# Optimization experiments

Hardware: AMD Instinct MI355X
Metric: run time of the kernel (lower is better)

Reference implementation:

```python
import jax, jax.numpy as jnp
import numpy as np

DIM = 512
HEADS = 8
DHEAD = DIM // 8          # 64
INNER = HEADS * DHEAD     # 512
M_LANDMARKS = 256
PINV_ITERS = 6
KSZ = 33                  # residual depthwise conv kernel (default)


def setup_inputs() -> dict:
    key = jax.random.key(0)
    ks = jax.random.split(key, 5)
    B, N = 1, 16384
    s = DIM ** -0.5
    return {
        "x": jax.random.normal(ks[0], (B, N, DIM), jnp.float32),
        "norm_w": jnp.ones((DIM,), jnp.float32),
        "norm_b": jnp.zeros((DIM,), jnp.float32),
        "w_qkv": jax.random.normal(ks[1], (3 * INNER, DIM), jnp.float32) * s,   # Linear(dim, 3*inner, bias=False)
        "w_out": jax.random.normal(ks[2], (DIM, INNER), jnp.float32) * s,        # Linear(inner, dim)
        "b_out": jnp.zeros((DIM,), jnp.float32),
        "conv_w": jax.random.normal(ks[3], (HEADS, 1, KSZ, 1), jnp.float32) * 0.1,  # depthwise Conv2d(h,h,(33,1),groups=h)
    }


def _layernorm(x, w, b, eps=1e-5):
    mu = x.mean(-1, keepdims=True)
    var = ((x - mu) ** 2).mean(-1, keepdims=True)
    return (x - mu) * jax.lax.rsqrt(var + eps) * w + b


def _moore_penrose_pinv(a, iters):
    # a: [B, H, m, m]; matches lucidrains moore_penrose_iter_pinv (global max over col/row sums)
    abs_a = jnp.abs(a)
    col = abs_a.sum(-1).max()
    row = abs_a.sum(-2).max()
    z = jnp.swapaxes(a, -1, -2) / (col * row)
    I = jnp.eye(a.shape[-1], dtype=a.dtype)
    for _ in range(iters):
        az = a @ z
        z = 0.25 * z @ (13 * I - az @ (15 * I - az @ (7 * I - az)))
    return z


def _nystrom_attention(h, w_qkv, w_out, b_out, conv_w):
    B, N, _ = h.shape
    qkv = h @ w_qkv.T                          # [B, N, 3*inner]
    q, k, v = jnp.split(qkv, 3, axis=-1)

    def heads(t):
        return t.reshape(B, N, HEADS, DHEAD).transpose(0, 2, 1, 3)  # [B, H, N, d]
    q = heads(q) * (DHEAD ** -0.5)
    k = heads(k)
    v = heads(v)

    # landmark pooling: mean over contiguous groups of size l = N / m
    l = N // M_LANDMARKS
    q_l = q.reshape(B, HEADS, M_LANDMARKS, l, DHEAD).mean(3)   # [B, H, m, d]
    k_l = k.reshape(B, HEADS, M_LANDMARKS, l, DHEAD).mean(3)

    attn1 = jax.nn.softmax(jnp.einsum('bhnd,bhmd->bhnm', q, k_l), axis=-1)      # [B,H,N,m]
    attn2 = jax.nn.softmax(jnp.einsum('bhid,bhjd->bhij', q_l, k_l), axis=-1)    # [B,H,m,m]
    attn3 = jax.nn.softmax(jnp.einsum('bhmd,bhnd->bhmn', q_l, k), axis=-1)      # [B,H,m,N]

    attn2_inv = _moore_penrose_pinv(attn2, PINV_ITERS)
    out = attn1 @ (attn2_inv @ (attn3 @ v))                                     # [B,H,N,d]

    # residual depthwise conv along sequence dim (kernel 33x1, groups=HEADS, no bias)
    conv = jax.lax.conv_general_dilated(
        v, conv_w, window_strides=(1, 1),
        padding=((KSZ // 2, KSZ // 2), (0, 0)),
        dimension_numbers=('NCHW', 'OIHW', 'NCHW'),
        feature_group_count=HEADS)
    out = out + conv

    out = out.transpose(0, 2, 1, 3).reshape(B, N, INNER)
    return out @ w_out.T + b_out


def reference(x, norm_w, norm_b, w_qkv, w_out, b_out, conv_w):
    h = _layernorm(x, norm_w, norm_b)
    return x + _nystrom_attention(h, w_qkv, w_out, b_out, conv_w)
```

## Files before the change

### kernel.cpp

```cpp
#include <hip/hip_runtime.h>
#include <hip/hip_bf16.h>


typedef __attribute__((ext_vector_type(8))) short bf16x8;
typedef __attribute__((ext_vector_type(4))) float f32x4;

#define MFMA16(A, B, C) __builtin_amdgcn_mfma_f32_16x16x32_bf16(A, B, C, 0, 0, 0)
#define GLD16(g, l) __builtin_amdgcn_global_load_lds( \
    (const __attribute__((address_space(1))) void*)(g), \
    (__attribute__((address_space(3))) void*)(l), 16, 0, 0)

static __device__ __forceinline__ unsigned short f2b(float f) {
  __hip_bfloat16 h = __float2bfloat16(f);
  return *reinterpret_cast<unsigned short*>(&h);
}
static __device__ __forceinline__ float b2f(unsigned short u) {
  return __uint_as_float(((unsigned)u) << 16);
}

#define FMA16(ACC, AV, BV) do { \
  ACC[0][0] += AV.x*BV.x; ACC[0][1] += AV.x*BV.y; ACC[0][2] += AV.x*BV.z; ACC[0][3] += AV.x*BV.w; \
  ACC[1][0] += AV.y*BV.x; ACC[1][1] += AV.y*BV.y; ACC[1][2] += AV.y*BV.z; ACC[1][3] += AV.y*BV.w; \
  ACC[2][0] += AV.z*BV.x; ACC[2][1] += AV.z*BV.y; ACC[2][2] += AV.z*BV.z; ACC[2][3] += AV.z*BV.w; \
  ACC[3][0] += AV.w*BV.x; ACC[3][1] += AV.w*BV.y; ACC[3][2] += AV.w*BV.z; ACC[3][3] += AV.w*BV.w; \
} while (0)

__global__ __launch_bounds__(256) void k_init(const float* __restrict__ x,
    const float* __restrict__ nw, const float* __restrict__ nb,
    unsigned short* __restrict__ h,
    const float* __restrict__ wq, unsigned short* __restrict__ wqb,
    const float* __restrict__ wo, unsigned short* __restrict__ wob) {
  const int b = blockIdx.x;
  const int t = threadIdx.x;
  if (b < 8192) {
    const int row = b * 2 + (t >> 7);
    const int tl = t & 127;
    const float4 xv = ((const float4*)(x + (size_t)row * 512))[tl];
    float s  = xv.x + xv.y + xv.z + xv.w;
    float sq = xv.x*xv.x + xv.y*xv.y + xv.z*xv.z + xv.w*xv.w;
    #pragma unroll
    for (int o = 32; o > 0; o >>= 1) {
      s  += __shfl_down(s, o, 64);
      sq += __shfl_down(sq, o, 64);
    }
    __shared__ float ls[4], lq[4];
    if ((t & 63) == 0) { ls[t >> 6] = s; lq[t >> 6] = sq; }
    __syncthreads();
    const int base = (t >> 7) << 1;
    s = ls[base] + ls[base + 1]; sq = lq[base] + lq[base + 1];
    const float mean = s * (1.0f / 512.0f);
    const float var  = sq * (1.0f / 512.0f) - mean * mean;
    const float rstd = rsqrtf(var + 1e-5f);
    const float4 wv = ((const float4*)nw)[tl];
    const float4 bv = ((const float4*)nb)[tl];
    ushort4 hv;
    hv.x = f2b((xv.x - mean) * rstd * wv.x + bv.x);
    hv.y = f2b((xv.y - mean) * rstd * wv.y + bv.y);
    hv.z = f2b((xv.z - mean) * rstd * wv.z + bv.z);
    hv.w = f2b((xv.w - mean) * rstd * wv.w + bv.w);
    ((ushort4*)(h + (size_t)row * 512))[tl] = hv;
  } else if (b < 8960) {
    const int i = (b - 8192) * 256 + t;
    const float4 f = ((const float4*)wq)[i];
    ushort4 u;
    u.x = f2b(f.x); u.y = f2b(f.y); u.z = f2b(f.z); u.w = f2b(f.w);
    ((ushort4*)wqb)[i] = u;
  } else {
    const int i = (b - 8960) * 256 + t;
    const float4 f = ((const float4*)wo)[i];
    ushort4 u;
    u.x = f2b(f.x); u.y = f2b(f.y); u.z = f2b(f.z); u.w = f2b(f.w);
    ((ushort4*)wob)[i] = u;
  }
}

__device__ __forceinline__ void stage_tile(const unsigned short* __restrict__ A,
    const unsigned short* __restrict__ B, unsigned short* lds,
    int m0, int n0, int k0, int tid) {
  #pragma unroll
  for (int c = 0; c < 2; ++c) {
    const int s = c * 512 + tid;
    const int grow = ((s >> 6) << 4) | (s & 15);
    const int chunk = (s >> 4) & 3;
    GLD16(A + (size_t)(m0 + grow) * 512 + k0 + chunk * 8, lds + s * 8);
    GLD16(B + (size_t)(n0 + grow) * 512 + k0 + chunk * 8, lds + 8192 + s * 8);
  }
}

__device__ __forceinline__ void compute_tile(const unsigned short* lds,
    f32x4 (&acc)[8][4], int wr, int wc, int quad, int l15) {
  bf16x8 a[8], b[4];
  #pragma unroll
  for (int i = 0; i < 8; ++i)
    a[i] = *(const bf16x8*)(lds + (size_t)((wr * 8 + i) * 64 + quad * 16 + l15) * 8);
  #pragma unroll
  for (int j = 0; j < 4; ++j)
    b[j] = *(const bf16x8*)(lds + 8192 + (size_t)((wc * 4 + j) * 64 + quad * 16 + l15) * 8);
  __builtin_amdgcn_s_setprio(1);
  #pragma unroll
  for (int i = 0; i < 8; ++i)
    #pragma unroll
    for (int j = 0; j < 4; ++j)
      acc[i][j] = MFMA16(a[i], b[j], acc[i][j]);
  __builtin_amdgcn_s_setprio(0);
}

#define GEMM256_PIPELINE(Aptr, Bptr, M0, N0)                                 \
  f32x4 acc[8][4];                                                           \
  _Pragma("unroll")                                                          \
  for (int i = 0; i < 8; ++i)                                                \
    _Pragma("unroll")                                                        \
    for (int j = 0; j < 4; ++j) acc[i][j] = (f32x4){0.f, 0.f, 0.f, 0.f};     \
  stage_tile(Aptr, Bptr, lds, M0, N0, 0, tid);                               \
  asm volatile("" ::: "memory");                                             \
  stage_tile(Aptr, Bptr, lds + 16384, M0, N0, 32, tid);                      \
  asm volatile("s_waitcnt vmcnt(4)" ::: "memory");                           \
  __builtin_amdgcn_s_barrier();                                              \
  for (int t = 0; t < 14; ++t) {                                             \
    compute_tile(lds + (t & 1) * 16384, acc, wr, wc, quad, l15);             \
    asm volatile("" ::: "memory");                                           \
    __builtin_amdgcn_s_barrier();       \
    asm volatile("" ::: "memory");                                           \
    stage_tile(Aptr, Bptr, lds + (t & 1) * 16384, M0, N0, (t + 2) * 32, tid);\
    asm volatile("s_waitcnt vmcnt(4)" ::: "memory");    \
    __builtin_amdgcn_s_barrier();                                            \
  }                                                                          \
  compute_tile(lds, acc, wr, wc, quad, l15);             \
  asm volatile("s_waitcnt vmcnt(0)" ::: "memory");                           \
  __builtin_amdgcn_s_barrier();                                              \
  compute_tile(lds + 16384, acc, wr, wc, quad, l15);

__global__ __launch_bounds__(512) void k_qkv2(const unsigned short* __restrict__ A,
    const unsigned short* __restrict__ B,
    unsigned short* __restrict__ qb, unsigned short* __restrict__ kb,
    unsigned short* __restrict__ vb) {
  __shared__ __align__(16) unsigned short lds[32768];
  const int tid = threadIdx.x;
  const int lane = tid & 63, w = tid >> 6;
  const int wr = w >> 2, wc = w & 3;
  const int quad = lane >> 4, l15 = lane & 15;
  const int bid = blockIdx.x;
  const int swz = (bid & 7) * 48 + (bid >> 3);
  const int by = swz / 6, bx = swz - by * 6;
  const int m0 = by * 256, n0 = bx * 256;

  GEMM256_PIPELINE(A, B, m0, n0)

  const int part = n0 >> 9;
  const int head = ((n0 & 511) >> 6) + wc;
  unsigned short* dst = (part == 0) ? qb : (part == 1) ? kb : vb;
  const float scale = (part == 0) ? 0.125f : 1.0f;
  unsigned short* dp = dst + (size_t)head * 16384 * 64;
  #pragma unroll
  for (int i = 0; i < 8; ++i) {
    const int rowb = m0 + wr * 128 + i * 16 + quad * 4;
    #pragma unroll
    for (int j = 0; j < 4; ++j) {
      const int dd = j * 16 + l15;
      #pragma unroll
      for (int r = 0; r < 4; ++r)
        dp[(size_t)(rowb + r) * 64 + dd] = f2b(acc[i][j][r] * scale);
    }
  }
}

__global__ __launch_bounds__(256) void k_tr(const unsigned short* __restrict__ v,
    unsigned short* __restrict__ vt) {
  __shared__ unsigned short T[64][72];
  const int t = threadIdx.x;
  const int n0 = blockIdx.x * 64, h = blockIdx.y;
  const int n = t >> 2, sg = (t & 3) * 16;
  const unsigned short* p = v + ((size_t)(h * 16384 + n0 + n)) * 64 + sg;
  #pragma unroll
  for (int i = 0; i < 16; i += 4) {
    const ushort4 u = *(const ushort4*)(p + i);
    T[sg + i + 0][n] = u.x; T[sg + i + 1][n] = u.y;
    T[sg + i + 2][n] = u.z; T[sg + i + 3][n] = u.w;
  }
  __syncthreads();
  const int d = t >> 2, so = (t & 3) * 16;
  unsigned short* q = vt + ((size_t)(h * 64 + d)) * 16384 + n0 + so;
  #pragma unroll
  for (int i = 0; i < 16; i += 4) {
    ushort4 u;
    u.x = T[d][so + i]; u.y = T[d][so + i + 1];
    u.z = T[d][so + i + 2]; u.w = T[d][so + i + 3];
    *(ushort4*)(q + i) = u;
  }
}

__global__ __launch_bounds__(256) void k_landmark(const unsigned short* __restrict__ qb,
    const unsigned short* __restrict__ kb, float* __restrict__ qlf,
    unsigned short* __restrict__ qlb, float* __restrict__ klf,
    unsigned short* __restrict__ klb) {
  const int t = threadIdx.x, d = t & 63, grp = t >> 6;
  const int m = blockIdx.x, h = blockIdx.y;
  const unsigned short* src = blockIdx.z ? kb : qb;
  const unsigned short* p = src + ((size_t)h * 16384 + m * 64 + grp * 16) * 64 + d;
  float s = 0.f;
  #pragma unroll
  for (int i = 0; i < 16; ++i) s += b2f(p[(size_t)i * 64]);
  __shared__ float red[4][64];
  red[grp][d] = s;
  __syncthreads();
  if (t < 64) {
    float v = (red[0][d] + red[1][d]) + (red[2][d] + red[3][d]);
    v *= (1.0f / 64.0f);
    const size_t oi = ((size_t)h * 256 + m) * 64 + d;
    if (blockIdx.z == 0) { qlf[oi] = v; qlb[oi] = f2b(v); }
    else                 { klf[oi] = v; klb[oi] = f2b(v); }
  }
}

__global__ __launch_bounds__(256) void k_attn2(const float* __restrict__ ql,
    const float* __restrict__ kl, float* __restrict__ a2, unsigned short* __restrict__ a2b,
    float* __restrict__ csum) {
  const int i = blockIdx.x, h = blockIdx.y, j = threadIdx.x;
  __shared__ float qrow[64];
  __shared__ float wred[4];
  __shared__ float wsum[4];
  if (j < 64) qrow[j] = ql[((size_t)h * 256 + i) * 64 + j];
  __syncthreads();
  const float* kr = kl + ((size_t)h * 256 + j) * 64;
  float s = 0.f;
  #pragma unroll 8
  for (int d = 0; d < 64; ++d) s += qrow[d] * kr[d];
  float mx = s;
  #pragma unroll
  for (int o2 = 32; o2 > 0; o2 >>= 1) mx = fmaxf(mx, __shfl_xor(mx, o2, 64));
  if ((j & 63) == 0) wred[j >> 6] = mx;
  __syncthreads();
  mx = fmaxf(fmaxf(wred[0], wred[1]), fmaxf(wred[2], wred[3]));
  const float e = __expf(s - mx);
  float sm = e;
  #pragma unroll
  for (int o2 = 32; o2 > 0; o2 >>= 1) sm += __shfl_xor(sm, o2, 64);
  if ((j & 63) == 0) wsum[j >> 6] = sm;
  __syncthreads();
  sm = wsum[0] + wsum[1] + wsum[2] + wsum[3];
  const float v = e / sm;
  const size_t idx = ((size_t)h * 256 + i) * 256 + j;
  a2[idx] = v;
  a2b[idx] = f2b(v);
  atomicAdd(&csum[h * 256 + j], v);
}

__global__ __launch_bounds__(256) void k_z0(const float* __restrict__ a2,
    const float* __restrict__ csum, unsigned short* __restrict__ z0b,
    unsigned short* __restrict__ z0t) {
  __shared__ float T[64][65];
  __shared__ float wm[4];
  const int bi = blockIdx.x, bj = blockIdx.y, h = blockIdx.z;
  const int t = threadIdx.x;
  const int r = t >> 2, cseg = (t & 3) * 16;
  float m = 0.f;
  #pragma unroll
  for (int c = 0; c < 8; ++c) m = fmaxf(m, csum[c * 256 + t]);
  #pragma unroll
  for (int o2 = 32; o2 > 0; o2 >>= 1) m = fmaxf(m, __shfl_xor(m, o2, 64));
  if ((t & 63) == 0) wm[t >> 6] = m;
  __syncthreads();
  const float g = fmaxf(fmaxf(wm[0], wm[1]), fmaxf(wm[2], wm[3]));
  const float inv = 1.0f / g;
  const float* p = a2 + ((size_t)h * 256 + bj * 64 + r) * 256 + bi * 64 + cseg;
  unsigned short* qt = z0t + ((size_t)h * 256 + bj * 64 + r) * 256 + bi * 64 + cseg;
  #pragma unroll
  for (int i = 0; i < 16; i += 4) {
    const float4 f = *(const float4*)(p + i);
    T[cseg + i + 0][r] = f.x; T[cseg + i + 1][r] = f.y;
    T[cseg + i + 2][r] = f.z; T[cseg + i + 3][r] = f.w;
    ushort4 u;
    u.x = f2b(f.x * inv); u.y = f2b(f.y * inv);
    u.z = f2b(f.z * inv); u.w = f2b(f.w * inv);
    *(ushort4*)(qt + i) = u;
  }
  __syncthreads();
  unsigned short* qb_ = z0b + ((size_t)h * 256 + bi * 64 + r) * 256 + bj * 64 + cseg;
  #pragma unroll
  for (int i = 0; i < 16; i += 4) {
    ushort4 u;
    u.x = f2b(T[r][cseg + i] * inv);     u.y = f2b(T[r][cseg + i + 1] * inv);
    u.z = f2b(T[r][cseg + i + 2] * inv); u.w = f2b(T[r][cseg + i + 3] * inv);
    *(ushort4*)(qb_ + i) = u;
  }
}

__global__ __launch_bounds__(256) void k_pgemm(const unsigned short* __restrict__ A,
    const unsigned short* __restrict__ Bt, unsigned short* __restrict__ Cn,
    unsigned short* __restrict__ Ct, float* __restrict__ Cf,
    float alpha, float sdiag, int use_diag) {
  __shared__ unsigned short As[64 * 128];
  __shared__ unsigned short Bs[64 * 128];
  const int t = threadIdx.x;
  const int lane = t & 63, w = t >> 6;
  const int quad = lane >> 4, l15 = lane & 15;
  const int bn = blockIdx.x, bm = blockIdx.y, h = blockIdx.z;
  const size_t hs = (size_t)h * 65536;
  const unsigned short* Ap = A + hs + (size_t)(bm * 64) * 256;
  const unsigned short* Bp = Bt + hs + (size_t)(bn * 64) * 256;
  f32x4 acc[4];
  #pragma unroll
  for (int j = 0; j < 4; ++j) acc[j] = (f32x4){0.f, 0.f, 0.f, 0.f};
  for (int kh = 0; kh < 2; ++kh) {
    __syncthreads();
    #pragma unroll
    for (int c = 0; c < 4; ++c) {
      const int slot = c * 256 + t;
      const int row = slot >> 4, pc = slot & 15;
      const int lc = pc ^ (row & 7);
      GLD16(Ap + (size_t)row * 256 + kh * 128 + lc * 8, As + slot * 8);
      GLD16(Bp + (size_t)row * 256 + kh * 128 + lc * 8, Bs + slot * 8);
    }
    __syncthreads();
    #pragma unroll
    for (int kc = 0; kc < 4; ++kc) {
      const int arow = w * 16 + l15;
      const bf16x8 a = *(const bf16x8*)(As + arow * 128 + ((kc * 4 + quad) ^ (arow & 7)) * 8);
      #pragma unroll
      for (int j = 0; j < 4; ++j) {
        const int brow = j * 16 + l15;
        const bf16x8 b = *(const bf16x8*)(Bs + brow * 128 + ((kc * 4 + quad) ^ (brow & 7)) * 8);
        acc[j] = MFMA16(a, b, acc[j]);
      }
    }
  }
  const int row0 = bm * 64 + w * 16 + quad * 4;
  #pragma unroll
  for (int j = 0; j < 4; ++j) {
    const int col = bn * 64 + j * 16 + l15;
    float v[4];
    #pragma unroll
    for (int r = 0; r < 4; ++r) v[r] = acc[j][r] * alpha;
    if (Cn) {
      #pragma unroll
      for (int r = 0; r < 4; ++r) Cn[hs + (size_t)(row0 + r) * 256 + col] = f2b(v[r]);
    }
    if (Cf) {
      #pragma unroll
      for (int r = 0; r < 4; ++r) Cf[hs + (size_t)(row0 + r) * 256 + col] = v[r];
    }
    ushort4 u;
    float tv[4];
    #pragma unroll
    for (int r = 0; r < 4; ++r)
      tv[r] = use_diag ? ((col == row0 + r ? sdiag : 0.f) - v[r]) : v[r];
    u.x = f2b(tv[0]); u.y = f2b(tv[1]); u.z = f2b(tv[2]); u.w = f2b(tv[3]);
    *(ushort4*)(Ct + hs + (size_t)col * 256 + row0) = u;
  }
}

__global__ __launch_bounds__(256) void k_gemm256(const float* __restrict__ A,
    const float* __restrict__ B, float* __restrict__ C,
    int lda, int ldb, int ldc,
    unsigned long long sA, unsigned long long sB, unsigned long long sC,
    float alpha, float sdiag, int use_diag,
    const float* __restrict__ rs, unsigned long long sRS) {
  A += (size_t)blockIdx.z * sA;
  B += (size_t)blockIdx.z * sB;
  C += (size_t)blockIdx.z * sC;
  if (rs) rs += (size_t)blockIdx.z * sRS;
  __shared__ float As[16][68];
  __shared__ float Bs[16][68];
  const int t = threadIdx.x, tx = t & 15, ty = t >> 4;
  const int bn = blockIdx.x, bm = blockIdx.y;
  const int lr = t >> 2, lk = (t & 3) << 2;
  const int bkr = t >> 4, bnc = (t & 15) << 2;
  float acc[4][4] = {{0.f}};
  for (int k0 = 0; k0 < 256; k0 += 16) {
    float4 a4 = *(const float4*)(A + (size_t)(bm * 64 + lr) * lda + k0 + lk);
    float4 b4 = *(const float4*)(B + (size_t)(k0 + bkr) * ldb + bn * 64 + bnc);
    if (use_diag) {
      const int kg = k0 + bkr, ngb = bn * 64 + bnc;
      b4.x = (kg == ngb + 0 ? sdiag : 0.f) - b4.x;
      b4.y = (kg == ngb + 1 ? sdiag : 0.f) - b4.y;
      b4.z = (kg == ngb + 2 ? sdiag : 0.f) - b4.z;
      b4.w = (kg == ngb + 3 ? sdiag : 0.f) - b4.w;
    }
    if (rs) {
      const float rv = 1.0f / rs[k0 + bkr];
      b4.x *= rv; b4.y *= rv; b4.z *= rv; b4.w *= rv;
    }
    __syncthreads();
    As[lk+0][lr] = a4.x; As[lk+1][lr] = a4.y; As[lk+2][lr] = a4.z; As[lk+3][lr] = a4.w;
    *(float4*)&Bs[bkr][bnc] = b4;
    __syncthreads();
    #pragma unroll
    for (int kq = 0; kq < 16; ++kq) {
      const float4 av = *(const float4*)&As[kq][ty << 2];
      const float4 bv = *(const float4*)&Bs[kq][tx << 2];
      FMA16(acc, av, bv);
    }
  }
  #pragma unroll
  for (int ii = 0; ii < 4; ++ii)
    #pragma unroll
    for (int jj = 0; jj < 4; ++jj)
      C[(size_t)(bm * 64 + (ty << 2) + ii) * ldc + bn * 64 + (tx << 2) + jj] =
          alpha * acc[ii][jj];
}

__global__ __launch_bounds__(256) void k_gemmD(const float* __restrict__ A,
    const float* __restrict__ B, const float* __restrict__ rs,
    unsigned short* __restrict__ dtb) {
  __shared__ float Asf[16 * 68];
  __shared__ float Bsf[16 * 68];
  const int bm = blockIdx.x, h = blockIdx.y;
  A += (size_t)h * 65536;
  B += (size_t)h * 16384;
  rs += (size_t)h * 256;
  const int t = threadIdx.x, tx = t & 15, ty = t >> 4;
  const int lr = t >> 2, lk = (t & 3) << 2;
  const int bkr = t >> 4, bnc = (t & 15) << 2;
  float acc[4][4] = {{0.f}};
  for (int k0 = 0; k0 < 256; k0 += 16) {
    float4 a4 = *(const float4*)(A + (size_t)(bm * 64 + lr) * 256 + k0 + lk);
    float4 b4 = *(const float4*)(B + (size_t)(k0 + bkr) * 64 + bnc);
    const float rv = 1.0f / rs[k0 + bkr];
    b4.x *= rv; b4.y *= rv; b4.z *= rv; b4.w *= rv;
    __syncthreads();
    Asf[(lk + 0) * 68 + lr] = a4.x; Asf[(lk + 1) * 68 + lr] = a4.y;
    Asf[(lk + 2) * 68 + lr] = a4.z; Asf[(lk + 3) * 68 + lr] = a4.w;
    *(float4*)&Bsf[bkr * 68 + bnc] = b4;
    __syncthreads();
    #pragma unroll
    for (int kq = 0; kq < 16; ++kq) {
      const float4 av = *(const float4*)&Asf[kq * 68 + (ty << 2)];
      const float4 bv = *(const float4*)&Bsf[kq * 68 + (tx << 2)];
      FMA16(acc, av, bv);
    }
  }
  #pragma unroll
  for (int ii = 0; ii < 4; ++ii)
    #pragma unroll
    for (int jj = 0; jj < 4; ++jj)
      dtb[(size_t)(h * 64 + (tx << 2) + jj) * 256 + bm * 64 + (ty << 2) + ii] =
          f2b(acc[ii][jj]);
}

__global__ __launch_bounds__(256) void k_w3_mfma(const unsigned short* __restrict__ qlb,
    const unsigned short* __restrict__ kb, const unsigned short* __restrict__ vt,
    float* __restrict__ W, float* __restrict__ lsum) {
  __shared__ unsigned short QLs[64 * 64];
  __shared__ unsigned short Ks [64 * 64];
  __shared__ unsigned short Vts[64 * 64];
  __shared__ unsigned short Ps [64 * 64];
  const int t = threadIdx.x;
  const int lane = t & 63, w = t >> 6;
  const int quad = lane >> 4, l15 = lane & 15;
  const int kc = blockIdx.x, mt = blockIdx.y, h = blockIdx.z;
  #pragma unroll
  for (int c = 0; c < 2; ++c) {
    const int slot = c * 256 + t;
    const int row = slot >> 3, pc = slot & 7, lc = pc ^ (row & 7);
    GLD16(qlb + ((size_t)(h * 256 + mt * 64 + row)) * 64 + lc * 8, QLs + slot * 8);
  }
  __syncthreads();
  const int arow = w * 16 + l15;
  const bf16x8 aq0 = *(const bf16x8*)(QLs + arow * 64 + ((quad    ) ^ (arow & 7)) * 8);
  const bf16x8 aq1 = *(const bf16x8*)(QLs + arow * 64 + ((quad + 4) ^ (arow & 7)) * 8);
  f32x4 wacc[4];
  #pragma unroll
  for (int dt = 0; dt < 4; ++dt) wacc[dt] = (f32x4){0.f, 0.f, 0.f, 0.f};
  float lacc[4] = {0.f, 0.f, 0.f, 0.f};
  for (int ss = 0; ss < 16; ++ss) {
    const int n0 = kc * 1024 + ss * 64;
    __syncthreads();
    #pragma unroll
    for (int c = 0; c < 2; ++c) {
      const int slot = c * 256 + t;
      const int row = slot >> 3, pc = slot & 7, lc = pc ^ (row & 7);
      GLD16(kb + ((size_t)(h * 16384 + n0 + row)) * 64 + lc * 8, Ks + slot * 8);
      GLD16(vt + ((size_t)(h * 64 + row)) * 16384 + n0 + lc * 8, Vts + slot * 8);
    }
    __syncthreads();
    f32x4 s[4];
    #pragma unroll
    for (int j = 0; j < 4; ++j) {
      s[j] = (f32x4){0.f, 0.f, 0.f, 0.f};
      const int brow = j * 16 + l15;
      const bf16x8 b0 = *(const bf16x8*)(Ks + brow * 64 + ((quad    ) ^ (brow & 7)) * 8);
      const bf16x8 b1 = *(const bf16x8*)(Ks + brow * 64 + ((quad + 4) ^ (brow & 7)) * 8);
      s[j] = MFMA16(aq0, b0, s[j]);
      s[j] = MFMA16(aq1, b1, s[j]);
    }
    #pragma unroll
    for (int j = 0; j < 4; ++j)
      #pragma unroll
      for (int r = 0; r < 4; ++r) {
        const float e = __expf(s[j][r]);
        lacc[r] += e;
        const int prow = w * 16 + quad * 4 + r, pcol = j * 16 + l15;
        Ps[prow * 64 + (((pcol >> 3) ^ (prow & 7)) << 3) + (pcol & 7)] = f2b(e);
      }
    __syncthreads();
    const bf16x8 ap0 = *(const bf16x8*)(Ps + arow * 64 + ((quad    ) ^ (arow & 7)) * 8);
    const bf16x8 ap1 = *(const bf16x8*)(Ps + arow * 64 + ((quad + 4) ^ (arow & 7)) * 8);
    #pragma unroll
    for (int dt = 0; dt < 4; ++dt) {
      const int brow = dt * 16 + l15;
      const bf16x8 b0 = *(const bf16x8*)(Vts + brow * 64 + ((quad    ) ^ (brow & 7)) * 8);
      const bf16x8 b1 = *(const bf16x8*)(Vts + brow * 64 + ((quad + 4) ^ (brow & 7)) * 8);
      wacc[dt] = MFMA16(ap0, b0, wacc[dt]);
      wacc[dt] = MFMA16(ap1, b1, wacc[dt]);
    }
  }
  #pragma unroll
  for (int dt = 0; dt < 4; ++dt)
    #pragma unroll
    for (int r = 0; r < 4; ++r)
      atomicAdd(&W[((size_t)(h * 256 + mt * 64 + w * 16 + quad * 4 + r)) * 64 + dt * 16 + l15],
                wacc[dt][r]);
// ... 47 lines not shown
  __syncthreads();
  f32x4 cacc[4];
  #pragma unroll
  for (int dt = 0; dt < 4; ++dt) cacc[dt] = (f32x4){0.f, 0.f, 0.f, 0.f};
  #pragma unroll
  for (int kcc = 0; kcc < 3; ++kcc) {
    const bf16x8 a = *(const bf16x8*)(Wb + arow * 96 + (((kcc * 4 + quad) ^ (arow & 3)) << 3));
    int off = n0 - 16 + kcc * 32 + quad * 8;
    off = off < 0 ? 0 : (off > 16376 ? 16376 : off);
    #pragma unroll
    for (int dt = 0; dt < 4; ++dt) {
      const bf16x8 b = *(const bf16x8*)(vt + ((size_t)(h * 64 + dt * 16 + l15)) * 16384 + off);
      cacc[dt] = MFMA16(a, b, cacc[dt]);
    }
  }
  f32x4 oacc[4];
  #pragma unroll
  for (int dt = 0; dt < 4; ++dt) oacc[dt] = (f32x4){0.f, 0.f, 0.f, 0.f};
  float lacc[4] = {0.f, 0.f, 0.f, 0.f};
  for (int mc = 0; mc < 4; ++mc) {
    const int m0 = mc * 64;
    __syncthreads();
    #pragma unroll
    for (int c = 0; c < 2; ++c) {
      const int slot = c * 256 + t;
      const int row = slot >> 3, pc = slot & 7, lc = pc ^ (row & 7);
      GLD16(klb + ((size_t)(h * 256 + m0 + row)) * 64 + lc * 8, Ks + slot * 8);
      GLD16(dtb + ((size_t)(h * 64 + row)) * 256 + m0 + lc * 8, Ds + slot * 8);
    }
    __syncthreads();
    f32x4 s[4];
    #pragma unroll
    for (int j = 0; j < 4; ++j) {
      s[j] = (f32x4){0.f, 0.f, 0.f, 0.f};
      const int brow = j * 16 + l15;
      const bf16x8 b0 = *(const bf16x8*)(Ks + brow * 64 + ((quad    ) ^ (brow & 7)) * 8);
      const bf16x8 b1 = *(const bf16x8*)(Ks + brow * 64 + ((quad + 4) ^ (brow & 7)) * 8);
      s[j] = MFMA16(aq0, b0, s[j]);
      s[j] = MFMA16(aq1, b1, s[j]);
    }
    #pragma unroll
    for (int j = 0; j < 4; ++j)
      #pragma unroll
      for (int r = 0; r < 4; ++r) {
        const float e = __expf(s[j][r]);
        lacc[r] += e;
        const int prow = w * 16 + quad * 4 + r, pcol = j * 16 + l15;
        Ps[prow * 64 + (((pcol >> 3) ^ (prow & 7)) << 3) + (pcol & 7)] = f2b(e);
      }
    __syncthreads();
    const bf16x8 ap0 = *(const bf16x8*)(Ps + arow * 64 + ((quad    ) ^ (arow & 7)) * 8);
    const bf16x8 ap1 = *(const bf16x8*)(Ps + arow * 64 + ((quad + 4) ^ (arow & 7)) * 8);
    #pragma unroll
    for (int dt = 0; dt < 4; ++dt) {
      const int brow = dt * 16 + l15;
      const bf16x8 b0 = *(const bf16x8*)(Ds + brow * 64 + ((quad    ) ^ (brow & 7)) * 8);
      const bf16x8 b1 = *(const bf16x8*)(Ds + brow * 64 + ((quad + 4) ^ (brow & 7)) * 8);
      oacc[dt] = MFMA16(ap0, b0, oacc[dt]);
      oacc[dt] = MFMA16(ap1, b1, oacc[dt]);
    }
  }
  #pragma unroll
  for (int r = 0; r < 4; ++r)
    #pragma unroll
    for (int msk = 1; msk < 16; msk <<= 1) lacc[r] += __shfl_xor(lacc[r], msk, 64);
  #pragma unroll
  for (int dt = 0; dt < 4; ++dt)
    #pragma unroll
    for (int r = 0; r < 4; ++r) {
      const float val = oacc[dt][r] / lacc[r] + cacc[dt][r];
      o[((size_t)(n0 + w * 16 + quad * 4 + r)) * 512 + h * 64 + dt * 16 + l15] = f2b(val);
    }
}

__global__ __launch_bounds__(256) void k_out_mfma(const unsigned short* __restrict__ A,
    const unsigned short* __restrict__ B, const float* __restrict__ bias,
    const float* __restrict__ xres, float* __restrict__ out) {
  __shared__ unsigned short As[128 * 32];
  __shared__ unsigned short Bs[128 * 32];
  const int t = threadIdx.x;
  const int lane = t & 63, w = t >> 6;
  const int quad = lane >> 4, l15 = lane & 15;
  const int wm = (w >> 1) * 64, wn = (w & 1) * 64;
  const int m0 = blockIdx.y * 128, n0 = blockIdx.x * 128;
  f32x4 acc[4][4];
  #pragma unroll
  for (int i = 0; i < 4; ++i)
    #pragma unroll
    for (int j = 0; j < 4; ++j) acc[i][j] = (f32x4){0.f, 0.f, 0.f, 0.f};
  for (int k0 = 0; k0 < 512; k0 += 32) {
    __syncthreads();
    #pragma unroll
    for (int c = 0; c < 2; ++c) {
      const int slot = c * 256 + t;
      const int row = slot >> 2, seg = slot & 3;
      GLD16(A + (size_t)(m0 + row) * 512 + k0 + seg * 8, As + slot * 8);
      GLD16(B + (size_t)(n0 + row) * 512 + k0 + seg * 8, Bs + slot * 8);
    }
    __syncthreads();
    bf16x8 a[4], b[4];
    #pragma unroll
    for (int i = 0; i < 4; ++i)
      a[i] = *(const bf16x8*)(As + (wm + i * 16 + l15) * 32 + quad * 8);
    #pragma unroll
    for (int j = 0; j < 4; ++j)
      b[j] = *(const bf16x8*)(Bs + (wn + j * 16 + l15) * 32 + quad * 8);
    #pragma unroll
    for (int i = 0; i < 4; ++i)
      #pragma unroll
      for (int j = 0; j < 4; ++j)
        acc[i][j] = MFMA16(a[i], b[j], acc[i][j]);
  }
  #pragma unroll
  for (int i = 0; i < 4; ++i)
    #pragma unroll
    for (int j = 0; j < 4; ++j)
      #pragma unroll
      for (int r = 0; r < 4; ++r) {
        const int row = m0 + wm + i * 16 + quad * 4 + r;
        const int col = n0 + wn + j * 16 + l15;
        out[(size_t)row * 512 + col] = acc[i][j][r] + bias[col] + xres[(size_t)row * 512 + col];
      }
}

extern "C" void kernel_launch(void* const* d_in, const int* in_sizes, int n_in,
                              void* d_out, int out_size, void* d_ws, size_t ws_size,
                              hipStream_t stream) {
  const float* x      = (const float*)d_in[0];
  const float* norm_w = (const float*)d_in[1];
  const float* norm_b = (const float*)d_in[2];
  const float* w_qkv  = (const float*)d_in[3];
  const float* w_out  = (const float*)d_in[4];
  const float* b_out  = (const float*)d_in[5];
  const float* conv_w = (const float*)d_in[6];
  float* out = (float*)d_out;

  char* cur = (char*)d_ws;
  auto alloc = [&](size_t bytes) -> char* {
    char* p = cur;
    cur += (bytes + 255) & ~(size_t)255;
    return p;
  };
  const size_t NB = (size_t)16384 * 512;
  const size_t LM = (size_t)8 * 256 * 64;
  const size_t SQ = (size_t)8 * 256 * 256;

  unsigned short* h_b  = (unsigned short*)alloc(NB * 2);
  unsigned short* wq_b = (unsigned short*)alloc((size_t)1536 * 512 * 2);
  unsigned short* wo_b = (unsigned short*)alloc((size_t)512 * 512 * 2);
  unsigned short* qb   = (unsigned short*)alloc(NB * 2);
  unsigned short* kb   = (unsigned short*)alloc(NB * 2);
  unsigned short* vb   = (unsigned short*)alloc(NB * 2);
  unsigned short* vt   = (unsigned short*)alloc(NB * 2);
  float*          qlf  = (float*)alloc(LM * 4);
  float*          klf  = (float*)alloc(LM * 4);
  unsigned short* qlb  = (unsigned short*)alloc(LM * 2);
  unsigned short* klb  = (unsigned short*)alloc(LM * 2);
  float*          a2   = (float*)alloc(SQ * 4);
  unsigned short* a2b  = (unsigned short*)alloc(SQ * 2);
  unsigned short* z0b  = (unsigned short*)alloc(SQ * 2);
  unsigned short* z0t  = (unsigned short*)alloc(SQ * 2);
  unsigned short* Pn   = (unsigned short*)alloc(SQ * 2);
  unsigned short* Pt   = (unsigned short*)alloc(SQ * 2);
  unsigned short* Q1t  = (unsigned short*)alloc(SQ * 2);
  unsigned short* Q2t  = (unsigned short*)alloc(SQ * 2);
  unsigned short* zp0n = (unsigned short*)alloc(SQ * 2);
  unsigned short* zp0t = (unsigned short*)alloc(SQ * 2);
  unsigned short* zp1n = (unsigned short*)alloc(SQ * 2);
  unsigned short* zp1t = (unsigned short*)alloc(SQ * 2);
  float*          zf5  = (float*)alloc(SQ * 4);
  float*          zfin = (float*)alloc(SQ * 4);
  float*          Pp   = (float*)alloc(SQ * 4);
  float*          Q1   = (float*)alloc(SQ * 4);
  float*          Q2   = (float*)alloc(SQ * 4);
  float*          W    = (float*)alloc(LM * 4 + 4096 * 4);
  float*          lsum = W + LM;
  float*          csum = W + LM + 2048;
  unsigned short* dtb  = (unsigned short*)alloc(LM * 2);
  unsigned short* o_b  = (unsigned short*)alloc(NB * 2);

  hipMemsetAsync(W, 0, (LM + 4096) * sizeof(float), stream);
  k_init<<<9216, 256, 0, stream>>>(x, norm_w, norm_b, h_b, w_qkv, wq_b, w_out, wo_b);
  k_qkv2<<<384, 512, 0, stream>>>(h_b, wq_b, qb, kb, vb);
  k_tr<<<dim3(256, 8), 256, 0, stream>>>(vb, vt);
  k_landmark<<<dim3(256, 8, 2), 256, 0, stream>>>(qb, kb, qlf, qlb, klf, klb);
  k_attn2<<<dim3(256, 8), 256, 0, stream>>>(qlf, klf, a2, a2b, csum);
  k_z0<<<dim3(4, 4, 8), 256, 0, stream>>>(a2, csum, z0b, z0t);
  k_w3_mfma<<<dim3(16, 4, 8), 256, 0, stream>>>(qlb, kb, vt, W, lsum);

  unsigned short* zan = z0b; unsigned short* zat = z0t;
  for (int it = 0; it < 5; ++it) {
    unsigned short* zbn = (it & 1) ? zp1n : zp0n;
    unsigned short* zbt = (it & 1) ? zp1t : zp0t;
    k_pgemm<<<dim3(4, 4, 8), 256, 0, stream>>>(a2b, zat, Pn, Pt, nullptr, 1.f, 7.f, 1);
    k_pgemm<<<dim3(4, 4, 8), 256, 0, stream>>>(Pn, Pt, nullptr, Q1t, nullptr, 1.f, 15.f, 1);
    k_pgemm<<<dim3(4, 4, 8), 256, 0, stream>>>(Pn, Q1t, nullptr, Q2t, nullptr, 1.f, 13.f, 1);
    k_pgemm<<<dim3(4, 4, 8), 256, 0, stream>>>(zan, Q2t, zbn, zbt,
        it == 4 ? zf5 : nullptr, 0.25f, 0.f, 0);
    zan = zbn; zat = zbt;
  }
  k_gemm256<<<dim3(4, 4, 8), 256, 0, stream>>>(a2, zf5, Pp, 256, 256, 256,
      65536ULL, 65536ULL, 65536ULL, 1.f, 0.f, 0, nullptr, 0ULL);
  k_gemm256<<<dim3(4, 4, 8), 256, 0, stream>>>(Pp, Pp, Q1, 256, 256, 256,
      65536ULL, 65536ULL, 65536ULL, 1.f, 7.f, 1, nullptr, 0ULL);
  k_gemm256<<<dim3(4, 4, 8), 256, 0, stream>>>(Pp, Q1, Q2, 256, 256, 256,
      65536ULL, 65536ULL, 65536ULL, 1.f, 15.f, 1, nullptr, 0ULL);
  k_gemm256<<<dim3(4, 4, 8), 256, 0, stream>>>(zf5, Q2, zfin, 256, 256, 256,
      65536ULL, 65536ULL, 65536ULL, 0.25f, 13.f, 1, nullptr, 0ULL);

  k_gemmD<<<dim3(4, 8), 256, 0, stream>>>(zfin, W, lsum, dtb);

  k_attn1_mfma<<<dim3(256, 8), 256, 0, stream>>>(qb, klb, dtb, vt, conv_w, o_b);
  k_out_mfma<<<dim3(4, 128), 256, 0, stream>>>(o_b, wo_b, b_out, x, out);
}
```

Before: 446.8 us.

## Retile QKV GEMM, fuse transpose with landmark pooling, halve pinv GEMM tiles

Replaces the 256x256 double-buffered QKV GEMM with a simpler 128x128 single-buffered MFMA kernel that uses an XCD-aware block mapping. The V transpose and the landmark pooling are merged into one launch. The pinv GEMMs (bf16 MFMA and fp32) switch to 64x32 tiles, doubling block count so the small matrices fill more CUs. The output GEMM gets an XCD-aware swizzle. The aim is more parallelism and fewer launches, at the cost of dropping the software pipelining in the largest GEMM.

```diff
diff --git a/kernel.cpp b/kernel.cpp
--- a/kernel.cpp
+++ b/kernel.cpp
@@ -17,13 +17,6 @@
 static __device__ __forceinline__ float b2f(unsigned short u) {
   return __uint_as_float(((unsigned)u) << 16);
 }
-
-#define FMA16(ACC, AV, BV) do { \
-  ACC[0][0] += AV.x*BV.x; ACC[0][1] += AV.x*BV.y; ACC[0][2] += AV.x*BV.z; ACC[0][3] += AV.x*BV.w; \
-  ACC[1][0] += AV.y*BV.x; ACC[1][1] += AV.y*BV.y; ACC[1][2] += AV.y*BV.z; ACC[1][3] += AV.y*BV.w; \
-  ACC[2][0] += AV.z*BV.x; ACC[2][1] += AV.z*BV.y; ACC[2][2] += AV.z*BV.z; ACC[2][3] += AV.z*BV.w; \
-  ACC[3][0] += AV.w*BV.x; ACC[3][1] += AV.w*BV.y; ACC[3][2] += AV.w*BV.z; ACC[3][3] += AV.w*BV.w; \
-} while (0)
 
 __global__ __launch_bounds__(256) void k_init(const float* __restrict__ x,
     const float* __restrict__ nw, const float* __restrict__ nb,
@@ -74,141 +67,114 @@
   }
 }
 
-__device__ __forceinline__ void stage_tile(const unsigned short* __restrict__ A,
-    const unsigned short* __restrict__ B, unsigned short* lds,
-    int m0, int n0, int k0, int tid) {
-  #pragma unroll
-  for (int c = 0; c < 2; ++c) {
-    const int s = c * 512 + tid;
-    const int grow = ((s >> 6) << 4) | (s & 15);
-    const int chunk = (s >> 4) & 3;
-    GLD16(A + (size_t)(m0 + grow) * 512 + k0 + chunk * 8, lds + s * 8);
-    GLD16(B + (size_t)(n0 + grow) * 512 + k0 + chunk * 8, lds + 8192 + s * 8);
-  }
-}
-
-__device__ __forceinline__ void compute_tile(const unsigned short* lds,
-    f32x4 (&acc)[8][4], int wr, int wc, int quad, int l15) {
-  bf16x8 a[8], b[4];
-  #pragma unroll
-  for (int i = 0; i < 8; ++i)
-    a[i] = *(const bf16x8*)(lds + (size_t)((wr * 8 + i) * 64 + quad * 16 + l15) * 8);
-  #pragma unroll
-  for (int j = 0; j < 4; ++j)
-    b[j] = *(const bf16x8*)(lds + 8192 + (size_t)((wc * 4 + j) * 64 + quad * 16 + l15) * 8);
-  __builtin_amdgcn_s_setprio(1);
-  #pragma unroll
-  for (int i = 0; i < 8; ++i)
-    #pragma unroll
-    for (int j = 0; j < 4; ++j)
-      acc[i][j] = MFMA16(a[i], b[j], acc[i][j]);
-  __builtin_amdgcn_s_setprio(0);
-}
-
-#define GEMM256_PIPELINE(Aptr, Bptr, M0, N0)                                 \
-  f32x4 acc[8][4];                                                           \
-  _Pragma("unroll")                                                          \
-  for (int i = 0; i < 8; ++i)                                                \
-    _Pragma("unroll")                                                        \
-    for (int j = 0; j < 4; ++j) acc[i][j] = (f32x4){0.f, 0.f, 0.f, 0.f};     \
-  stage_tile(Aptr, Bptr, lds, M0, N0, 0, tid);                               \
-  asm volatile("" ::: "memory");                                             \
-  stage_tile(Aptr, Bptr, lds + 16384, M0, N0, 32, tid);                      \
-  asm volatile("s_waitcnt vmcnt(4)" ::: "memory");                           \
-  __builtin_amdgcn_s_barrier();                                              \
-  for (int t = 0; t < 14; ++t) {                                             \
-    compute_tile(lds + (t & 1) * 16384, acc, wr, wc, quad, l15);             \
-    asm volatile("" ::: "memory");                                           \
-    __builtin_amdgcn_s_barrier();       \
-    asm volatile("" ::: "memory");                                           \
-    stage_tile(Aptr, Bptr, lds + (t & 1) * 16384, M0, N0, (t + 2) * 32, tid);\
-    asm volatile("s_waitcnt vmcnt(4)" ::: "memory");    \
-    __builtin_amdgcn_s_barrier();                                            \
-  }                                                                          \
-  compute_tile(lds, acc, wr, wc, quad, l15);             \
-  asm volatile("s_waitcnt vmcnt(0)" ::: "memory");                           \
-  __builtin_amdgcn_s_barrier();                                              \
-  compute_tile(lds + 16384, acc, wr, wc, quad, l15);
-
-__global__ __launch_bounds__(512) void k_qkv2(const unsigned short* __restrict__ A,
+__global__ __launch_bounds__(256) void k_qkv_mfma(const unsigned short* __restrict__ A,
     const unsigned short* __restrict__ B,
     unsigned short* __restrict__ qb, unsigned short* __restrict__ kb,
     unsigned short* __restrict__ vb) {
-  __shared__ __align__(16) unsigned short lds[32768];
-  const int tid = threadIdx.x;
-  const int lane = tid & 63, w = tid >> 6;
-  const int wr = w >> 2, wc = w & 3;
+  __shared__ unsigned short As[128 * 32];
+  __shared__ unsigned short Bs[128 * 32];
+  const int t = threadIdx.x;
+  const int lane = t & 63, w = t >> 6;
   const int quad = lane >> 4, l15 = lane & 15;
+  const int wm = (w >> 1) * 64, wn = (w & 1) * 64;
   const int bid = blockIdx.x;
-  const int swz = (bid & 7) * 48 + (bid >> 3);
-  const int by = swz / 6, bx = swz - by * 6;
-  const int m0 = by * 256, n0 = bx * 256;
-
-  GEMM256_PIPELINE(A, B, m0, n0)
-
+  const int xcd = bid & 7, i0 = bid >> 3;
+  const int by = xcd * 16 + i0 / 12, bx = i0 % 12;
+  const int m0 = by * 128, n0 = bx * 128;
+  f32x4 acc[4][4];
+  #pragma unroll
+  for (int i = 0; i < 4; ++i)
+    #pragma unroll
+    for (int j = 0; j < 4; ++j) acc[i][j] = (f32x4){0.f, 0.f, 0.f, 0.f};
+  for (int k0 = 0; k0 < 512; k0 += 32) {
+    __syncthreads();
+    #pragma unroll
+    for (int c = 0; c < 2; ++c) {
+      const int slot = c * 256 + t;
+      const int row = slot >> 2, seg = slot & 3;
+      GLD16(A + (size_t)(m0 + row) * 512 + k0 + seg * 8, As + slot * 8);
+      GLD16(B + (size_t)(n0 + row) * 512 + k0 + seg * 8, Bs + slot * 8);
+    }
+    __syncthreads();
+    bf16x8 a[4], b[4];
+    #pragma unroll
+    for (int i = 0; i < 4; ++i)
+      a[i] = *(const bf16x8*)(As + (wm + i * 16 + l15) * 32 + quad * 8);
+    #pragma unroll
+    for (int j = 0; j < 4; ++j)
+      b[j] = *(const bf16x8*)(Bs + (wn + j * 16 + l15) * 32 + quad * 8);
+    #pragma unroll
+    for (int i = 0; i < 4; ++i)
+      #pragma unroll
+      for (int j = 0; j < 4; ++j)
+        acc[i][j] = MFMA16(a[i], b[j], acc[i][j]);
+  }
   const int part = n0 >> 9;
-  const int head = ((n0 & 511) >> 6) + wc;
-  unsigned short* dst = (part == 0) ? qb : (part == 1) ? kb : vb;
-  const float scale = (part == 0) ? 0.125f : 1.0f;
-  unsigned short* dp = dst + (size_t)head * 16384 * 64;
-  #pragma unroll
-  for (int i = 0; i < 8; ++i) {
-    const int rowb = m0 + wr * 128 + i * 16 + quad * 4;
-    #pragma unroll
-    for (int j = 0; j < 4; ++j) {
-      const int dd = j * 16 + l15;
+  #pragma unroll
+  for (int i = 0; i < 4; ++i)
+    #pragma unroll
+    for (int j = 0; j < 4; ++j)
       #pragma unroll
-      for (int r = 0; r < 4; ++r)
-        dp[(size_t)(rowb + r) * 64 + dd] = f2b(acc[i][j][r] * scale);
-    }
-  }
-}
-
-__global__ __launch_bounds__(256) void k_tr(const unsigned short* __restrict__ v,
-    unsigned short* __restrict__ vt) {
-  __shared__ unsigned short T[64][72];
-  const int t = threadIdx.x;
-  const int n0 = blockIdx.x * 64, h = blockIdx.y;
-  const int n = t >> 2, sg = (t & 3) * 16;
-  const unsigned short* p = v + ((size_t)(h * 16384 + n0 + n)) * 64 + sg;
-  #pragma unroll
-  for (int i = 0; i < 16; i += 4) {
-    const ushort4 u = *(const ushort4*)(p + i);
-    T[sg + i + 0][n] = u.x; T[sg + i + 1][n] = u.y;
-    T[sg + i + 2][n] = u.z; T[sg + i + 3][n] = u.w;
-  }
-  __syncthreads();
-  const int d = t >> 2, so = (t & 3) * 16;
-  unsigned short* q = vt + ((size_t)(h * 64 + d)) * 16384 + n0 + so;
-  #pragma unroll
-  for (int i = 0; i < 16; i += 4) {
-    ushort4 u;
-    u.x = T[d][so + i]; u.y = T[d][so + i + 1];
-    u.z = T[d][so + i + 2]; u.w = T[d][so + i + 3];
-    *(ushort4*)(q + i) = u;
-  }
-}
-
-__global__ __launch_bounds__(256) void k_landmark(const unsigned short* __restrict__ qb,
+      for (int r = 0; r < 4; ++r) {
+        const int row = m0 + wm + i * 16 + quad * 4 + r;
+        const int col = n0 + wn + j * 16 + l15;
+        const int rem = col & 511;
+        const int hd = rem >> 6, dd = rem & 63;
+        const size_t idx = ((size_t)hd * 16384 + row) * 64 + dd;
+        const float val = acc[i][j][r];
+        if (part == 0)      qb[idx] = f2b(val * 0.125f);
+        else if (part == 1) kb[idx] = f2b(val);
+        else                vb[idx] = f2b(val);
+      }
+}
+
+__global__ __launch_bounds__(256) void k_prep(const unsigned short* __restrict__ vb,
+    unsigned short* __restrict__ vt, const unsigned short* __restrict__ qb,
     const unsigned short* __restrict__ kb, float* __restrict__ qlf,
     unsigned short* __restrict__ qlb, float* __restrict__ klf,
     unsigned short* __restrict__ klb) {
-  const int t = threadIdx.x, d = t & 63, grp = t >> 6;
-  const int m = blockIdx.x, h = blockIdx.y;
-  const unsigned short* src = blockIdx.z ? kb : qb;
-  const unsigned short* p = src + ((size_t)h * 16384 + m * 64 + grp * 16) * 64 + d;
-  float s = 0.f;
-  #pragma unroll
-  for (int i = 0; i < 16; ++i) s += b2f(p[(size_t)i * 64]);
-  __shared__ float red[4][64];
-  red[grp][d] = s;
-  __syncthreads();
-  if (t < 64) {
-    float v = (red[0][d] + red[1][d]) + (red[2][d] + red[3][d]);
-    v *= (1.0f / 64.0f);
-    const size_t oi = ((size_t)h * 256 + m) * 64 + d;
-    if (blockIdx.z == 0) { qlf[oi] = v; qlb[oi] = f2b(v); }
-    else                 { klf[oi] = v; klb[oi] = f2b(v); }
+  __shared__ __align__(16) unsigned char smem[64 * 72 * 2];
+  const int t = threadIdx.x;
+  const int h = blockIdx.y;
+  if (blockIdx.z == 0) {
+    auto T = (unsigned short(*)[72])smem;
+    const int n0 = blockIdx.x * 64;
+    const int n = t >> 2, sg = (t & 3) * 16;
+    const unsigned short* p = vb + ((size_t)(h * 16384 + n0 + n)) * 64 + sg;
+    #pragma unroll
+    for (int i = 0; i < 16; i += 4) {
+      const ushort4 u = *(const ushort4*)(p + i);
+      T[sg + i + 0][n] = u.x; T[sg + i + 1][n] = u.y;
+      T[sg + i + 2][n] = u.z; T[sg + i + 3][n] = u.w;
+    }
+    __syncthreads();
+    const int d = t >> 2, so = (t & 3) * 16;
+    unsigned short* q = vt + ((size_t)(h * 64 + d)) * 16384 + n0 + so;
+    #pragma unroll
+    for (int i = 0; i < 16; i += 4) {
+      ushort4 u;
+      u.x = T[d][so + i]; u.y = T[d][so + i + 1];
+      u.z = T[d][so + i + 2]; u.w = T[d][so + i + 3];
+      *(ushort4*)(q + i) = u;
+    }
+  } else {
+    auto red = (float(*)[64])smem;
+    const int d = t & 63, grp = t >> 6;
+    const int m = blockIdx.x;
+    const unsigned short* src = (blockIdx.z == 1) ? qb : kb;
+    const unsigned short* p = src + ((size_t)h * 16384 + m * 64 + grp * 16) * 64 + d;
+    float s = 0.f;
+    #pragma unroll
+    for (int i = 0; i < 16; ++i) s += b2f(p[(size_t)i * 64]);
+    red[grp][d] = s;
+    __syncthreads();
+    if (t < 64) {
+      float v = (red[0][d] + red[1][d]) + (red[2][d] + red[3][d]);
+      v *= (1.0f / 64.0f);
+      const size_t oi = ((size_t)h * 256 + m) * 64 + d;
+      if (blockIdx.z == 1) { qlf[oi] = v; qlb[oi] = f2b(v); }
+      else                 { klf[oi] = v; klb[oi] = f2b(v); }
+    }
   }
 }
 
@@ -289,45 +255,48 @@
     const unsigned short* __restrict__ Bt, unsigned short* __restrict__ Cn,
     unsigned short* __restrict__ Ct, float* __restrict__ Cf,
     float alpha, float sdiag, int use_diag) {
-  __shared__ unsigned short As[64 * 128];
-  __shared__ unsigned short Bs[64 * 128];
+  __shared__ unsigned short As[64 * 256];
+  __shared__ unsigned short Bs[32 * 256];
   const int t = threadIdx.x;
   const int lane = t & 63, w = t >> 6;
   const int quad = lane >> 4, l15 = lane & 15;
   const int bn = blockIdx.x, bm = blockIdx.y, h = blockIdx.z;
   const size_t hs = (size_t)h * 65536;
   const unsigned short* Ap = A + hs + (size_t)(bm * 64) * 256;
-  const unsigned short* Bp = Bt + hs + (size_t)(bn * 64) * 256;
-  f32x4 acc[4];
-  #pragma unroll
-  for (int j = 0; j < 4; ++j) acc[j] = (f32x4){0.f, 0.f, 0.f, 0.f};
-  for (int kh = 0; kh < 2; ++kh) {
-    __syncthreads();
-    #pragma unroll
-    for (int c = 0; c < 4; ++c) {
-      const int slot = c * 256 + t;
-      const int row = slot >> 4, pc = slot & 15;
-      const int lc = pc ^ (row & 7);
-      GLD16(Ap + (size_t)row * 256 + kh * 128 + lc * 8, As + slot * 8);
-      GLD16(Bp + (size_t)row * 256 + kh * 128 + lc * 8, Bs + slot * 8);
-    }
-    __syncthreads();
-    #pragma unroll
-    for (int kc = 0; kc < 4; ++kc) {
-      const int arow = w * 16 + l15;
-      const bf16x8 a = *(const bf16x8*)(As + arow * 128 + ((kc * 4 + quad) ^ (arow & 7)) * 8);
-      #pragma unroll
-      for (int j = 0; j < 4; ++j) {
-        const int brow = j * 16 + l15;
-        const bf16x8 b = *(const bf16x8*)(Bs + brow * 128 + ((kc * 4 + quad) ^ (brow & 7)) * 8);
-        acc[j] = MFMA16(a, b, acc[j]);
-      }
+  const unsigned short* Bp = Bt + hs + (size_t)(bn * 32) * 256;
+  #pragma unroll
+  for (int c = 0; c < 8; ++c) {
+    const int s = c * 256 + t;
+    const int row = s >> 5, pc = s & 31;
+    const int lc = pc ^ (row & 7);
+    GLD16(Ap + (size_t)row * 256 + lc * 8, As + s * 8);
+  }
+  #pragma unroll
+  for (int c = 0; c < 4; ++c) {
+    const int s = c * 256 + t;
+    const int row = s >> 5, pc = s & 31;
+    const int lc = pc ^ (row & 7);
+    GLD16(Bp + (size_t)row * 256 + lc * 8, Bs + s * 8);
+  }
+  f32x4 acc[2];
+  acc[0] = (f32x4){0.f, 0.f, 0.f, 0.f};
+  acc[1] = (f32x4){0.f, 0.f, 0.f, 0.f};
+  __syncthreads();
+  const int arow = w * 16 + l15;
+  #pragma unroll
+  for (int kc = 0; kc < 8; ++kc) {
+    const bf16x8 a = *(const bf16x8*)(As + arow * 256 + (((kc * 4 + quad) ^ (arow & 7)) * 8));
+    #pragma unroll
+    for (int j = 0; j < 2; ++j) {
+      const int brow = j * 16 + l15;
+      const bf16x8 b = *(const bf16x8*)(Bs + brow * 256 + (((kc * 4 + quad) ^ (brow & 7)) * 8));
+      acc[j] = MFMA16(a, b, acc[j]);
     }
   }
   const int row0 = bm * 64 + w * 16 + quad * 4;
   #pragma unroll
-  for (int j = 0; j < 4; ++j) {
-    const int col = bn * 64 + j * 16 + l15;
+  for (int j = 0; j < 2; ++j) {
+    const int col = bn * 32 + j * 16 + l15;
     float v[4];
     #pragma unroll
     for (int r = 0; r < 4; ++r) v[r] = acc[j][r] * alpha;
@@ -351,51 +320,44 @@
 
 __global__ __launch_bounds__(256) void k_gemm256(const float* __restrict__ A,
     const float* __restrict__ B, float* __restrict__ C,
-    int lda, int ldb, int ldc,
-    unsigned long long sA, unsigned long long sB, unsigned long long sC,
-    float alpha, float sdiag, int use_diag,
-    const float* __restrict__ rs, unsigned long long sRS) {
-  A += (size_t)blockIdx.z * sA;
-  B += (size_t)blockIdx.z * sB;
-  C += (size_t)blockIdx.z * sC;
-  if (rs) rs += (size_t)blockIdx.z * sRS;
+    float alpha, float sdiag, int use_diag) {
+  A += (size_t)blockIdx.z * 65536;
+  B += (size_t)blockIdx.z * 65536;
+  C += (size_t)blockIdx.z * 65536;
   __shared__ float As[16][68];
-  __shared__ float Bs[16][68];
+  __shared__ float Bs[16][36];
   const int t = threadIdx.x, tx = t & 15, ty = t >> 4;
   const int bn = blockIdx.x, bm = blockIdx.y;
   const int lr = t >> 2, lk = (t & 3) << 2;
-  const int bkr = t >> 4, bnc = (t & 15) << 2;
-  float acc[4][4] = {{0.f}};
+  const int bkr = t >> 4, bnc = (t & 15) << 1;
+  float acc[4][2] = {{0.f}};
   for (int k0 = 0; k0 < 256; k0 += 16) {
-    float4 a4 = *(const float4*)(A + (size_t)(bm * 64 + lr) * lda + k0 + lk);
-    float4 b4 = *(const float4*)(B + (size_t)(k0 + bkr) * ldb + bn * 64 + bnc);
+    float4 a4 = *(const float4*)(A + (size_t)(bm * 64 + lr) * 256 + k0 + lk);
+    float2 b2 = *(const float2*)(B + (size_t)(k0 + bkr) * 256 + bn * 32 + bnc);
     if (use_diag) {
-      const int kg = k0 + bkr, ngb = bn * 64 + bnc;
-      b4.x = (kg == ngb + 0 ? sdiag : 0.f) - b4.x;
-      b4.y = (kg == ngb + 1 ? sdiag : 0.f) - b4.y;
-      b4.z = (kg == ngb + 2 ? sdiag : 0.f) - b4.z;
-      b4.w = (kg == ngb + 3 ? sdiag : 0.f) - b4.w;
-    }
-    if (rs) {
-      const float rv = 1.0f / rs[k0 + bkr];
-      b4.x *= rv; b4.y *= rv; b4.z *= rv; b4.w *= rv;
+      const int kg = k0 + bkr, ngb = bn * 32 + bnc;
+      b2.x = (kg == ngb + 0 ? sdiag : 0.f) - b2.x;
+      b2.y = (kg == ngb + 1 ? sdiag : 0.f) - b2.y;
     }
     __syncthreads();
     As[lk+0][lr] = a4.x; As[lk+1][lr] = a4.y; As[lk+2][lr] = a4.z; As[lk+3][lr] = a4.w;
-    *(float4*)&Bs[bkr][bnc] = b4;
+    Bs[bkr][bnc] = b2.x; Bs[bkr][bnc + 1] = b2.y;
     __syncthreads();
     #pragma unroll
     for (int kq = 0; kq < 16; ++kq) {
       const float4 av = *(const float4*)&As[kq][ty << 2];
-      const float4 bv = *(const float4*)&Bs[kq][tx << 2];
-      FMA16(acc, av, bv);
+      const float bx_ = Bs[kq][tx << 1], by_ = Bs[kq][(tx << 1) + 1];
+      acc[0][0] += av.x * bx_; acc[0][1] += av.x * by_;
+      acc[1][0] += av.y * bx_; acc[1][1] += av.y * by_;
+      acc[2][0] += av.z * bx_; acc[2][1] += av.z * by_;
+      acc[3][0] += av.w * bx_; acc[3][1] += av.w * by_;
     }
   }
   #pragma unroll
   for (int ii = 0; ii < 4; ++ii)
     #pragma unroll
-    for (int jj = 0; jj < 4; ++jj)
-      C[(size_t)(bm * 64 + (ty << 2) + ii) * ldc + bn * 64 + (tx << 2) + jj] =
+    for (int jj = 0; jj < 2; ++jj)
+      C[(size_t)(bm * 64 + (ty << 2) + ii) * 256 + bn * 32 + (tx << 1) + jj] =
           alpha * acc[ii][jj];
 }
 
@@ -426,7 +388,10 @@
     for (int kq = 0; kq < 16; ++kq) {
       const float4 av = *(const float4*)&Asf[kq * 68 + (ty << 2)];
       const float4 bv = *(const float4*)&Bsf[kq * 68 + (tx << 2)];
-      FMA16(acc, av, bv);
+      acc[0][0] += av.x*bv.x; acc[0][1] += av.x*bv.y; acc[0][2] += av.x*bv.z; acc[0][3] += av.x*bv.w;
+      acc[1][0] += av.y*bv.x; acc[1][1] += av.y*bv.y; acc[1][2] += av.y*bv.z; acc[1][3] += av.y*bv.w;
+      acc[2][0] += av.z*bv.x; acc[2][1] += av.z*bv.y; acc[2][2] += av.z*bv.z; acc[2][3] += av.z*bv.w;
+      acc[3][0] += av.w*bv.x; acc[3][1] += av.w*bv.y; acc[3][2] += av.w*bv.z; acc[3][3] += av.w*bv.w;
     }
   }
   #pragma unroll
@@ -640,7 +605,10 @@
   const int lane = t & 63, w = t >> 6;
   const int quad = lane >> 4, l15 = lane & 15;
   const int wm = (w >> 1) * 64, wn = (w & 1) * 64;
-  const int m0 = blockIdx.y * 128, n0 = blockIdx.x * 128;
+  const int bid = blockIdx.x;
+  const int xcd = bid & 7, i0 = bid >> 3;
+  const int by = xcd * 16 + (i0 >> 2), bx = i0 & 3;
+  const int m0 = by * 128, n0 = bx * 128;
   f32x4 acc[4][4];
   #pragma unroll
   for (int i = 0; i < 4; ++i)
@@ -739,9 +707,8 @@
 
   hipMemsetAsync(W, 0, (LM + 4096) * sizeof(float), stream);
   k_init<<<9216, 256, 0, stream>>>(x, norm_w, norm_b, h_b, w_qkv, wq_b, w_out, wo_b);
-  k_qkv2<<<384, 512, 0, stream>>>(h_b, wq_b, qb, kb, vb);
-  k_tr<<<dim3(256, 8), 256, 0, stream>>>(vb, vt);
-  k_landmark<<<dim3(256, 8, 2), 256, 0, stream>>>(qb, kb, qlf, qlb, klf, klb);
+  k_qkv_mfma<<<1536, 256, 0, stream>>>(h_b, wq_b, qb, kb, vb);
+  k_prep<<<dim3(256, 8, 3), 256, 0, stream>>>(vb, vt, qb, kb, qlf, qlb, klf, klb);
   k_attn2<<<dim3(256, 8), 256, 0, stream>>>(qlf, klf, a2, a2b, csum);
   k_z0<<<dim3(4, 4, 8), 256, 0, stream>>>(a2, csum, z0b, z0t);
   k_w3_mfma<<<dim3(16, 4, 8), 256, 0, stream>>>(qlb, kb, vt, W, lsum);
@@ -750,24 +717,20 @@
   for (int it = 0; it < 5; ++it) {
     unsigned short* zbn = (it & 1) ? zp1n : zp0n;
     unsigned short* zbt = (it & 1) ? zp1t : zp0t;
-    k_pgemm<<<dim3(4, 4, 8), 256, 0, stream>>>(a2b, zat, Pn, Pt, nullptr, 1.f, 7.f, 1);
-    k_pgemm<<<dim3(4, 4, 8), 256, 0, stream>>>(Pn, Pt, nullptr, Q1t, nullptr, 1.f, 15.f, 1);
-    k_pgemm<<<dim3(4, 4, 8), 256, 0, stream>>>(Pn, Q1t, nullptr, Q2t, nullptr, 1.f, 13.f, 1);
-    k_pgemm<<<dim3(4, 4, 8), 256, 0, stream>>>(zan, Q2t, zbn, zbt,
+    k_pgemm<<<dim3(8, 4, 8), 256, 0, stream>>>(a2b, zat, Pn, Pt, nullptr, 1.f, 7.f, 1);
+    k_pgemm<<<dim3(8, 4, 8), 256, 0, stream>>>(Pn, Pt, nullptr, Q1t, nullptr, 1.f, 15.f, 1);
+    k_pgemm<<<dim3(8, 4, 8), 256, 0, stream>>>(Pn, Q1t, nullptr, Q2t, nullptr, 1.f, 13.f, 1);
+    k_pgemm<<<dim3(8, 4, 8), 256, 0, stream>>>(zan, Q2t, zbn, zbt,
         it == 4 ? zf5 : nullptr, 0.25f, 0.f, 0);
     zan = zbn; zat = zbt;
   }
-  k_gemm256<<<dim3(4, 4, 8), 256, 0, stream>>>(a2, zf5, Pp, 256, 256, 256,
-      65536ULL, 65536ULL, 65536ULL, 1.f, 0.f, 0, nullptr, 0ULL);
-  k_gemm256<<<dim3(4, 4, 8), 256, 0, stream>>>(Pp, Pp, Q1, 256, 256, 256,
-      65536ULL, 65536ULL, 65536ULL, 1.f, 7.f, 1, nullptr, 0ULL);
-  k_gemm256<<<dim3(4, 4, 8), 256, 0, stream>>>(Pp, Q1, Q2, 256, 256, 256,
-      65536ULL, 65536ULL, 65536ULL, 1.f, 15.f, 1, nullptr, 0ULL);
-  k_gemm256<<<dim3(4, 4, 8), 256, 0, stream>>>(zf5, Q2, zfin, 256, 256, 256,
-      65536ULL, 65536ULL, 65536ULL, 0.25f, 13.f, 1, nullptr, 0ULL);
+  k_gemm256<<<dim3(8, 4, 8), 256, 0, stream>>>(a2, zf5, Pp, 1.f, 0.f, 0);
+  k_gemm256<<<dim3(8, 4, 8), 256, 0, stream>>>(Pp, Pp, Q1, 1.f, 7.f, 1);
+  k_gemm256<<<dim3(8, 4, 8), 256, 0, stream>>>(Pp, Q1, Q2, 1.f, 15.f, 1);
+  k_gemm256<<<dim3(8, 4, 8), 256, 0, stream>>>(zf5, Q2, zfin, 0.25f, 13.f, 1);
 
   k_gemmD<<<dim3(4, 8), 256, 0, stream>>>(zfin, W, lsum, dtb);
 
   k_attn1_mfma<<<dim3(256, 8), 256, 0, stream>>>(qb, klb, dtb, vt, conv_w, o_b);
-  k_out_mfma<<<dim3(4, 128), 256, 0, stream>>>(o_b, wo_b, b_out, x, out);
-}
+  k_out_mfma<<<512, 256, 0, stream>>>(o_b, wo_b, b_out, x, out);
+}
```

New measurement: 410.6 us. 1.09x faster.
